# Performance work log

Measured on AMD Instinct MI355X. Metric: run time of the kernel, lower is better.

Reference implementation:

```python
import jax, jax.numpy as jnp
import numpy as np

RES, RES_, STRIDE = 28, 14, 2
H, KD, AR = 8, 16, 4
SCALE = KD ** -0.5
EPS = 1e-5


def make_bias_idxs(res=RES, res_=RES_, stride=STRIDE):
    pts = [(i, j) for i in range(res) for j in range(res)]
    pts_ = [(i, j) for i in range(res_) for j in range(res_)]
    offs, idxs = {}, []
    for p1 in pts_:
        for p2 in pts:
            off = (abs(p1[0] * stride - p2[0]), abs(p1[1] * stride - p2[1]))
            if off not in offs:
                offs[off] = len(offs)
            idxs.append(offs[off])
    return np.array(idxs, dtype=np.int32).reshape(len(pts_), len(pts)), len(offs)


def setup_inputs() -> dict:
    key = jax.random.key(0)
    ks = jax.random.split(key, 16)
    idxs, n_off = make_bias_idxs()  # n_off == 784
    B, N, C = 128, RES * RES, 256
    d_kv, d_q, d_p, d_pin = 640, 128, 384, 512
    return {
        "hidden_state": jax.random.normal(ks[0], (B, N, C), jnp.float32),
        "w_kv": jax.random.normal(ks[1], (d_kv, C), jnp.float32) * 0.05,
        "kv_gamma": jax.random.uniform(ks[2], (d_kv,), jnp.float32, 0.5, 1.5),
        "kv_beta": jax.random.normal(ks[3], (d_kv,), jnp.float32) * 0.1,
        "kv_mean": jax.random.normal(ks[4], (d_kv,), jnp.float32) * 0.1,
        "kv_var": jax.random.uniform(ks[5], (d_kv,), jnp.float32, 0.5, 1.5),
        "w_q": jax.random.normal(ks[6], (d_q, C), jnp.float32) * 0.05,
        "q_gamma": jax.random.uniform(ks[7], (d_q,), jnp.float32, 0.5, 1.5),
        "q_beta": jax.random.normal(ks[8], (d_q,), jnp.float32) * 0.1,
        "q_mean": jax.random.normal(ks[9], (d_q,), jnp.float32) * 0.1,
        "q_var": jax.random.uniform(ks[10], (d_q,), jnp.float32, 0.5, 1.5),
        "w_proj": jax.random.normal(ks[11], (d_p, d_pin), jnp.float32) * 0.05,
        "p_gamma": jax.random.uniform(ks[12], (d_p,), jnp.float32, 0.5, 1.5),
        "p_beta": jax.random.normal(ks[13], (d_p,), jnp.float32) * 0.1,
        "p_mean": jax.random.normal(ks[14], (d_p,), jnp.float32) * 0.1,
        "p_var": jax.random.uniform(ks[15], (d_p,), jnp.float32, 0.5, 1.5),
        "attention_biases": jax.random.normal(jax.random.fold_in(key, 99), (H, n_off), jnp.float32),
        "attention_bias_idxs": jnp.asarray(idxs),
    }


def _bn(x, gamma, beta, mean, var):
    # eval-mode BatchNorm1d over last dim
    return (x - mean) * (gamma * jax.lax.rsqrt(var + EPS)) + beta


def _hardswish(x):
    return x * jnp.clip(x + 3.0, 0.0, 6.0) * (1.0 / 6.0)


def reference(hidden_state, w_kv, kv_gamma, kv_beta, kv_mean, kv_var,
              w_q, q_gamma, q_beta, q_mean, q_var,
              w_proj, p_gamma, p_beta, p_mean, p_var,
              attention_biases, attention_bias_idxs):
    B, N, C = hidden_state.shape
    N_ = RES_ * RES_
    # kv: [B, N, 640] -> key [B,H,N,KD], value [B,H,N,AR*KD]
    kv = _bn(hidden_state @ w_kv.T, kv_gamma, kv_beta, kv_mean, kv_var)
    kv = kv.reshape(B, N, H, KD + AR * KD)
    k = jnp.transpose(kv[..., :KD], (0, 2, 1, 3))          # [B,H,N,KD]
    v = jnp.transpose(kv[..., KD:], (0, 2, 1, 3))          # [B,H,N,AR*KD]
    # strided query subsample on the spatial grid
    hs = hidden_state.reshape(B, RES, RES, C)[:, ::STRIDE, ::STRIDE].reshape(B, N_, C)
    q = _bn(hs @ w_q.T, q_gamma, q_beta, q_mean, q_var)
    q = jnp.transpose(q.reshape(B, N_, H, KD), (0, 2, 1, 3))  # [B,H,N_,KD]
    bias = attention_biases[:, attention_bias_idxs]           # [H,N_,N] gathered
    attn = jnp.einsum('bhqd,bhkd->bhqk', q, k) * SCALE + bias
    attn = jax.nn.softmax(attn, axis=-1)
    out = jnp.einsum('bhqk,bhkd->bhqd', attn, v)              # [B,H,N_,AR*KD]
    out = jnp.transpose(out, (0, 2, 1, 3)).reshape(B, N_, H * AR * KD)
    out = _bn(_hardswish(out) @ w_proj.T, p_gamma, p_beta, p_mean, p_var)
    return out
```

## Files before the change

### kernel.cpp

```cpp
#include <hip/hip_runtime.h>

typedef _Float16 f16;
typedef __attribute__((ext_vector_type(2))) _Float16 f16x2;
typedef __attribute__((ext_vector_type(4))) _Float16 f16x4;
typedef __attribute__((ext_vector_type(8))) _Float16 f16x8;
typedef __attribute__((ext_vector_type(4))) float fvec4;
typedef __attribute__((ext_vector_type(4))) float f32x4;
typedef __attribute__((ext_vector_type(16))) float f32x16;
typedef __attribute__((ext_vector_type(4))) unsigned int uint4v;

#define NKEY 784
#define NKEYP 800
#define NQ 196
#define NQP 224
#define LOG2E 1.442695041f
#define SC2   0.360673760f
#define THR2  11.5415603f

static __device__ __forceinline__ f32x4 mfma16(f16x8 a, f16x8 b, f32x4 c) {
    return __builtin_amdgcn_mfma_f32_16x16x32_f16(a, b, c, 0, 0, 0);
}
static __device__ __forceinline__ f32x16 mfma32(f16x8 a, f16x8 b, f32x16 c) {
    return __builtin_amdgcn_mfma_f32_32x32x16_f16(a, b, c, 0, 0, 0);
}
static __device__ __forceinline__ unsigned pkrtz(float a, float b) {
    return __builtin_bit_cast(unsigned, __builtin_amdgcn_cvt_pkrtz(a, b));
}
static __device__ __forceinline__ f32x16 z16() {
    f32x16 v;
#pragma unroll
    for (int i = 0; i < 16; ++i) v[i] = 0.f;
    return v;
}
static __device__ __forceinline__ f32x16 load_ci(const float* p) {
    fvec4 c0 = *(const fvec4*)(p);
    fvec4 c1 = *(const fvec4*)(p + 256);
    fvec4 c2 = *(const fvec4*)(p + 512);
    fvec4 c3 = *(const fvec4*)(p + 768);
    f32x16 ci;
    ci[0] = c0[0];  ci[1] = c0[1];  ci[2] = c0[2];  ci[3] = c0[3];
    ci[4] = c1[0];  ci[5] = c1[1];  ci[6] = c1[2];  ci[7] = c1[3];
    ci[8] = c2[0];  ci[9] = c2[1];  ci[10] = c2[2]; ci[11] = c2[3];
    ci[12] = c3[0]; ci[13] = c3[1]; ci[14] = c3[2]; ci[15] = c3[3];
    return ci;
}

__global__ void prep_scales_all(const float* __restrict__ kg, const float* __restrict__ kb,
                                const float* __restrict__ km, const float* __restrict__ kvv,
                                const float* __restrict__ qg, const float* __restrict__ qb,
                                const float* __restrict__ qm, const float* __restrict__ qv,
                                const float* __restrict__ pg, const float* __restrict__ pb,
                                const float* __restrict__ pm, const float* __restrict__ pv,
                                float* __restrict__ sb) {
    int i = blockIdx.x * 256 + threadIdx.x;
    if (i < 640) {
        float s = kg[i] * rsqrtf(kvv[i] + 1e-5f);
        sb[i] = s; sb[640 + i] = kb[i] - km[i] * s;
    } else if (i < 768) {
        int j = i - 640;
        float s = qg[j] * rsqrtf(qv[j] + 1e-5f);
        sb[1280 + j] = s * SC2;
        sb[1408 + j] = (qb[j] - qm[j] * s) * SC2;
    } else if (i < 1152) {
        int j = i - 768;
        float s = pg[j] * rsqrtf(pv[j] + 1e-5f);
        sb[1536 + j] = s; sb[1920 + j] = pb[j] - pm[j] * s;
    }
}

__global__ void conv_w(const float* __restrict__ wkv, const float* __restrict__ wq,
                       const float* __restrict__ wp, f16* __restrict__ out) {
    int i = blockIdx.x * 256 + threadIdx.x;
    const float* src;
    f16* dst;
    int kc, n, K;
    if (i < 20480)      { int j = i;         kc = j / 640, n = j - kc * 640; src = wkv; dst = out + (size_t)j * 8;            K = 256; }
    else if (i < 24576) { int j = i - 20480; kc = j / 128, n = j - kc * 128; src = wq;  dst = out + 163840 + (size_t)j * 8;   K = 256; }
    else                { int j = i - 24576; kc = j / 384, n = j - kc * 384; src = wp;  dst = out + 196608 + (size_t)j * 8;   K = 512; }
    const float* s = src + (size_t)n * K + kc * 8;
    fvec4 v0 = *(const fvec4*)s;
    fvec4 v1 = *(const fvec4*)(s + 4);
    f16x8 h;
    h[0] = (f16)v0[0]; h[1] = (f16)v0[1]; h[2] = (f16)v0[2]; h[3] = (f16)v0[3];
    h[4] = (f16)v1[0]; h[5] = (f16)v1[1]; h[6] = (f16)v1[2]; h[7] = (f16)v1[3];
    *(f16x8*)dst = h;
}

__global__ void prep_bias(const float* __restrict__ biases, const int* __restrict__ idxs,
                          float* __restrict__ biasC, int n_off) {
    int tid = blockIdx.x * 256 + threadIdx.x;
    const int rj = tid & 3;
    const int lane = (tid >> 2) & 63;
    const int rr = (tid >> 8) & 3;
    const int g = tid >> 10;
    const int r = rr * 4 + rj;
    const int kbk = g % 25;
    const int tmp = g / 25;
    const int qt = tmp % 7;
    const int h = tmp / 7;
    const int q = qt * 32 + (lane & 31);
    const int key = kbk * 32 + (r & 3) + 8 * (r >> 2) + 4 * (lane >> 5);
    float v;
    if (key >= NKEY)  v = -1e30f;
    else if (q < NQ)  v = biases[h * n_off + idxs[q * NKEY + key]] * LOG2E;
    else              v = 0.f;
    biasC[tid] = v;
}

template <int MODE>
__global__ __launch_bounds__(256) void gemm_db(
        const void* __restrict__ Ap, const f16x8* __restrict__ Wg,
        const float* __restrict__ sc, const float* __restrict__ sh,
        void* __restrict__ OutA, f16* __restrict__ OutV) {
    constexpr int K     = (MODE == 2) ? 512 : 256;
    constexpr int KS    = K / 32;
    constexpr int CHUNK = (MODE == 2) ? 16 : 32;
    constexpr int NFR   = CHUNK / 16;
    constexpr int NT    = (MODE == 0) ? 640 : (MODE == 1 ? 128 : 384);
    constexpr int NCH   = (MODE == 0) ? 20 : (MODE == 1 ? 4 : 12);
    constexpr int UNITS = (K / 8) * CHUNK;
    constexpr int SR    = UNITS / 256;

    __shared__ f16x8 Wl[2][UNITS];

    const int t = threadIdx.x;
    const int lane = t & 63, wid = t >> 6;
    const int fr = lane & 15, kg = lane >> 4;
    const int m0 = blockIdx.x * 64;
    const int nb0 = blockIdx.y * (NCH * CHUNK);
    const int mrow = m0 + wid * 16 + fr;

    size_t arow;
    if constexpr (MODE == 1) {
        int b = mrow / 196, nn = mrow - b * 196;
        arow = (size_t)b * 784 + (nn / 14) * 56 + (nn % 14) * 2;
    } else {
        arow = (size_t)mrow;
    }
    f16x8 af[KS];
#pragma unroll
    for (int ks = 0; ks < KS; ++ks) {
        if constexpr (MODE == 2) {
            af[ks] = *(const f16x8*)((const f16*)Ap + arow * K + ks * 32 + kg * 8);
        } else {
            const float* a = (const float*)Ap + arow * 256 + ks * 32 + kg * 8;
            fvec4 v0 = *(const fvec4*)a;
            fvec4 v1 = *(const fvec4*)(a + 4);
            f16x8 hv;
            hv[0] = (f16)v0[0]; hv[1] = (f16)v0[1]; hv[2] = (f16)v0[2]; hv[3] = (f16)v0[3];
            hv[4] = (f16)v1[0]; hv[5] = (f16)v1[1]; hv[6] = (f16)v1[2]; hv[7] = (f16)v1[3];
            af[ks] = hv;
        }
    }

#pragma unroll
    for (int rr = 0; rr < SR; ++rr) {
        const int idx = rr * 256 + t;
        Wl[0][idx] = Wg[(size_t)(idx / CHUNK) * NT + nb0 + (idx % CHUNK)];
    }
    __syncthreads();

    const int rg = kg * 4;
    int cur = 0;
    for (int c = 0; c < NCH; ++c) {
        const int n0c = nb0 + c * CHUNK;

        f16x8 nx0, nx1, nx2, nx3;
        if (c + 1 < NCH) {
            const int n0n = n0c + CHUNK;
            nx0 = Wg[(size_t)((0 * 256 + t) / CHUNK) * NT + n0n + ((0 * 256 + t) % CHUNK)];
            if constexpr (SR > 1)
                nx1 = Wg[(size_t)((1 * 256 + t) / CHUNK) * NT + n0n + ((1 * 256 + t) % CHUNK)];
            if constexpr (SR > 2) {
                nx2 = Wg[(size_t)((2 * 256 + t) / CHUNK) * NT + n0n + ((2 * 256 + t) % CHUNK)];
                nx3 = Wg[(size_t)((3 * 256 + t) / CHUNK) * NT + n0n + ((3 * 256 + t) % CHUNK)];
            }
        }

        f32x4 acc[NFR];
#pragma unroll
        for (int j = 0; j < NFR; ++j) acc[j] = (f32x4){0.f, 0.f, 0.f, 0.f};
#pragma unroll
        for (int ks = 0; ks < KS; ++ks) {
            f16x8 bfr[NFR];
#pragma unroll
            for (int nf = 0; nf < NFR; ++nf)
                bfr[nf] = Wl[cur][(ks * 4 + kg) * CHUNK + nf * 16 + fr];
#pragma unroll
            for (int nf = 0; nf < NFR; ++nf)
                acc[nf] = mfma16(af[ks], bfr[nf], acc[nf]);
        }

        const int mbase = m0 + wid * 16 + rg;
#pragma unroll
        for (int nf = 0; nf < NFR; ++nf) {
            const int n = n0c + nf * 16 + fr;
            const float scn = sc[n], shn = sh[n];
            if constexpr (MODE == 0) {
                const int b = mbase / 784;
                const int nn = mbase - b * 784;
                const int hd = n / 80;
                const int cc = n - hd * 80;
                const size_t bh = (size_t)(b * 8 + hd);
                if (cc < 16) {
#pragma unroll
                    for (int r = 0; r < 4; ++r) {
                        float y = acc[nf][r] * scn + shn;
                        ((f16*)OutA)[(bh * NKEYP + nn + r) * 16 + cc] = (f16)y;
                    }
                } else {
                    const int kbk = nn >> 5, sH = (nn >> 4) & 1;
                    const int kq = (nn >> 2) & 3;
                    const int slot = ((((kq & 1) << 1) | (kq >> 1)) << 2) | (nn & 3);
                    f16x4 pv;
#pragma unroll
                    for (int r = 0; r < 4; ++r) pv[r] = (f16)(acc[nf][r] * scn + shn);
                    *(f16x4*)(OutV + ((bh * 25 + kbk) * 2 + sH) * 1024 + (cc - 16) * 16 + slot) = pv;
                }
            } else if constexpr (MODE == 1) {
                const int b = mbase / 196;
                const int nn = mbase - b * 196;
                const int hd = n >> 4, cc = n & 15;
                const size_t bh = (size_t)(b * 8 + hd);
#pragma unroll
                for (int r = 0; r < 4; ++r) {
                    float y = acc[nf][r] * scn + shn;
                    ((f16*)OutA)[(bh * NQP + nn + r) * 16 + cc] = (f16)y;
                }
            } else {
#pragma unroll
                for (int r = 0; r < 4; ++r) {
                    float y = acc[nf][r] * scn + shn;
                    ((float*)OutA)[(size_t)(mbase + r) * 384 + n] = y;
                }
            }
        }

        if (c + 1 < NCH) {
            Wl[cur ^ 1][0 * 256 + t] = nx0;
            if constexpr (SR > 1)
                Wl[cur ^ 1][1 * 256 + t] = nx1;
            if constexpr (SR > 2) {
                Wl[cur ^ 1][2 * 256 + t] = nx2;
                Wl[cur ^ 1][3 * 256 + t] = nx3;
            }
            __syncthreads();
            cur ^= 1;
        }
    }
}

__global__ __launch_bounds__(64) void attn_fused(const f16* __restrict__ kb,
                                                 const f16* __restrict__ vtb,
                                                 const f16* __restrict__ qw,
                                                 const float* __restrict__ biasC,
                                                 f16* __restrict__ ao) {
    const int wg = blockIdx.x;
    const int x = wg & 7, p = wg >> 3;
    const int qt = p % 7;
    const int bh = (p / 7) * 8 + x;
    const int b = bh >> 3, h = bh & 7;
    const int lane = threadIdx.x;
    const int l31 = lane & 31;
    const int hh = lane >> 5;
    const int q0 = qt * 32;

    const f16x8 bq = *(const f16x8*)(qw + ((size_t)bh * NQP + q0 + l31) * 16 + hh * 8);
    const f16*   kpp = kb + (size_t)bh * (NKEYP * 16) + (size_t)l31 * 16 + hh * 8;
    const float* cbp = biasC + (size_t)(h * 7 + qt) * 25 * 1024 + lane * 4;
    const f16*   vkb = vtb + (size_t)bh * 51200 + l31 * 16 + hh * 8;

    float mrun = -1e30f;
    float lsum = 0.f;
    f32x16 o0 = z16(), o1 = z16();

    f32x16 sn = mfma32(*(const f16x8*)kpp, bq, load_ci(cbp));

#pragma unroll 1
    for (int kbi = 0; kbi < 25; ++kbi) {
        f32x16 s = sn;
        if (kbi + 1 < 25) {
            kpp += 512; cbp += 1024;
            sn = mfma32(*(const f16x8*)kpp, bq, load_ci(cbp));
        }
        f16x8 bv00 = *(const f16x8*)(vkb);
        f16x8 bv01 = *(const f16x8*)(vkb + 512);
        f16x8 bv10 = *(const f16x8*)(vkb + 1024);
        f16x8 bv11 = *(const f16x8*)(vkb + 1536);
        vkb += 2048;

        float m0v = fmaxf(fmaxf(s[0], s[1]), fmaxf(s[2], s[3]));
        float m1v = fmaxf(fmaxf(s[4], s[5]), fmaxf(s[6], s[7]));
        float m2v = fmaxf(fmaxf(s[8], s[9]), fmaxf(s[10], s[11]));
        float m3v = fmaxf(fmaxf(s[12], s[13]), fmaxf(s[14], s[15]));
        float cmax = fmaxf(fmaxf(m0v, m1v), fmaxf(m2v, m3v));
        cmax = fmaxf(cmax, __shfl_xor(cmax, 32));
        if (__any(cmax > mrun + THR2)) {
            float mnew = fmaxf(mrun, cmax);
            float f = exp2f(mrun - mnew);
            mrun = mnew;
            lsum *= f;
#pragma unroll
            for (int r = 0; r < 16; ++r) {
                const int cr = (r & 3) + ((r >> 2) << 3) + (hh << 2);
                float fr2 = __shfl(f, cr);
                o0[r] *= fr2;
                o1[r] *= fr2;
            }
        }
        float pr[16];
        float psum = 0.f;
#pragma unroll
        for (int r = 0; r < 16; ++r) {
            pr[r] = exp2f(s[r] - mrun);
            psum += pr[r];
        }
        lsum += psum;
        uint4v w0, w1;
        w0[0] = pkrtz(pr[0], pr[1]);   w0[1] = pkrtz(pr[2], pr[3]);
        w0[2] = pkrtz(pr[4], pr[5]);   w0[3] = pkrtz(pr[6], pr[7]);
        w1[0] = pkrtz(pr[8], pr[9]);   w1[1] = pkrtz(pr[10], pr[11]);
        w1[2] = pkrtz(pr[12], pr[13]); w1[3] = pkrtz(pr[14], pr[15]);
        f16x8 pa0 = __builtin_bit_cast(f16x8, w0);
        f16x8 pa1 = __builtin_bit_cast(f16x8, w1);
        o0 = mfma32(pa0, bv00, o0);
        o1 = mfma32(pa0, bv01, o1);
        o0 = mfma32(pa1, bv10, o0);
        o1 = mfma32(pa1, bv11, o1);
    }
    lsum += __shfl_xor(lsum, 32);
    const float inv = 1.0f / lsum;
#pragma unroll
    for (int r = 0; r < 16; ++r) {
        const int cr = (r & 3) + ((r >> 2) << 3) + (hh << 2);
        const float iq = __shfl(inv, cr);
        const int qg = q0 + cr;
        if (qg < NQ) {
            float v0 = o0[r] * iq, v1 = o1[r] * iq;
            float h0 = v0 * fminf(fmaxf(v0 + 3.f, 0.f), 6.f) * (1.f / 6.f);
            float h1 = v1 * fminf(fmaxf(v1 + 3.f, 0.f), 6.f) * (1.f / 6.f);
            f16* dst = ao + ((size_t)b * NQ + qg) * 512 + h * 64 + l31;
            dst[0] = (f16)h0;
            dst[32] = (f16)h1;
        }
    }
}

extern "C" void kernel_launch(void* const* d_in, const int* in_sizes, int n_in,
                              void* d_out, int out_size, void* d_ws, size_t ws_size,
                              hipStream_t stream) {
    (void)n_in; (void)out_size;
    const float* hidden = (const float*)d_in[0];
    const float* w_kv   = (const float*)d_in[1];
    const float* w_q    = (const float*)d_in[6];
    const float* w_p    = (const float*)d_in[11];
    const float* biases = (const float*)d_in[16];
    const int*   idxs   = (const int*)d_in[17];
    const int n_off = in_sizes[16] / 8;

    char* ws = (char*)d_ws;
    const size_t OFF_K  = 0;
    const size_t OFF_V  = 26214400;
    const size_t OFF_Q  = 131072000;
    const size_t OFF_AO = 138412032;
    const size_t OFF_W  = 164102144;
    const size_t OFF_SC = 164888576;
    const size_t OFF_BT = 164897792;
    const size_t NEED   = OFF_BT + 5734400;
    f16*   kbuf  = (f16*)(ws + OFF_K);
    f16*   vbuf  = (f16*)(ws + OFF_V);
    f16*   qbuf  = (f16*)(ws + OFF_Q);
    f16*   aobuf = (f16*)(ws + OFF_AO);
    f16*   wf16  = (f16*)(ws + OFF_W);
    float* scbuf = (float*)(ws + OFF_SC);
    float* btbuf = (ws_size >= NEED) ? (float*)(ws + OFF_BT) : (float*)d_out;

    prep_scales_all<<<5, 256, 0, stream>>>(
        (const float*)d_in[2], (const float*)d_in[3], (const float*)d_in[4], (const float*)d_in[5],
        (const float*)d_in[7], (const float*)d_in[8], (const float*)d_in[9], (const float*)d_in[10],
        (const float*)d_in[12], (const float*)d_in[13], (const float*)d_in[14], (const float*)d_in[15],
        scbuf);
    conv_w<<<192, 256, 0, stream>>>(w_kv, w_q, w_p, wf16);
    prep_bias<<<5600, 256, 0, stream>>>(biases, idxs, btbuf, n_off);
    hipMemsetAsync(qbuf, 0, (size_t)1024 * NQP * 16 * 2, stream);
    gemm_db<0><<<dim3(1568, 1), 256, 0, stream>>>(hidden, (const f16x8*)wf16, scbuf, scbuf + 640, kbuf, vbuf);
    gemm_db<1><<<dim3(392, 1), 256, 0, stream>>>(hidden, (const f16x8*)(wf16 + 163840), scbuf + 1280, scbuf + 1408, qbuf, nullptr);
    attn_fused<<<7168, 64, 0, stream>>>(kbuf, vbuf, qbuf, btbuf, aobuf);
    gemm_db<2><<<dim3(392, 2), 256, 0, stream>>>(aobuf, (const f16x8*)(wf16 + 196608), scbuf + 1536, scbuf + 1920, d_out, nullptr);
}
```

Before: 226.9 us.

## Store attention bias as fp16 and run all query tiles of a head in one block

The precomputed bias table becomes fp16 with a per-lane contiguous layout, so each lane loads it as two 16-byte vectors instead of four strided float4 loads, halving bias traffic. The attention kernel now launches one 448-thread block per batch-head, with seven waves covering the query tiles, so K and V loads for a head are shared through cache within a block. The fp16 bias loses precision, and the padding mask value changes to -30000. The fallback that wrote the bias table into the output buffer when workspace was small is removed.

```diff
diff --git a/kernel.cpp b/kernel.cpp
--- a/kernel.cpp
+++ b/kernel.cpp
@@ -31,18 +31,6 @@
 #pragma unroll
     for (int i = 0; i < 16; ++i) v[i] = 0.f;
     return v;
-}
-static __device__ __forceinline__ f32x16 load_ci(const float* p) {
-    fvec4 c0 = *(const fvec4*)(p);
-    fvec4 c1 = *(const fvec4*)(p + 256);
-    fvec4 c2 = *(const fvec4*)(p + 512);
-    fvec4 c3 = *(const fvec4*)(p + 768);
-    f32x16 ci;
-    ci[0] = c0[0];  ci[1] = c0[1];  ci[2] = c0[2];  ci[3] = c0[3];
-    ci[4] = c1[0];  ci[5] = c1[1];  ci[6] = c1[2];  ci[7] = c1[3];
-    ci[8] = c2[0];  ci[9] = c2[1];  ci[10] = c2[2]; ci[11] = c2[3];
-    ci[12] = c3[0]; ci[13] = c3[1]; ci[14] = c3[2]; ci[15] = c3[3];
-    return ci;
 }
 
 __global__ void prep_scales_all(const float* __restrict__ kg, const float* __restrict__ kb,
@@ -87,13 +75,11 @@
 }
 
 __global__ void prep_bias(const float* __restrict__ biases, const int* __restrict__ idxs,
-                          float* __restrict__ biasC, int n_off) {
+                          f16* __restrict__ biasS, int n_off) {
     int tid = blockIdx.x * 256 + threadIdx.x;
-    const int rj = tid & 3;
-    const int lane = (tid >> 2) & 63;
-    const int rr = (tid >> 8) & 3;
+    const int r = tid & 15;
+    const int lane = (tid >> 4) & 63;
     const int g = tid >> 10;
-    const int r = rr * 4 + rj;
     const int kbk = g % 25;
     const int tmp = g / 25;
     const int qt = tmp % 7;
@@ -101,10 +87,10 @@
     const int q = qt * 32 + (lane & 31);
     const int key = kbk * 32 + (r & 3) + 8 * (r >> 2) + 4 * (lane >> 5);
     float v;
-    if (key >= NKEY)  v = -1e30f;
+    if (key >= NKEY)  v = -30000.f;
     else if (q < NQ)  v = biases[h * n_off + idxs[q * NKEY + key]] * LOG2E;
     else              v = 0.f;
-    biasC[tid] = v;
+    biasS[tid] = (f16)v;
 }
 
 template <int MODE>
@@ -250,38 +236,49 @@
     }
 }
 
-__global__ __launch_bounds__(64) void attn_fused(const f16* __restrict__ kb,
-                                                 const f16* __restrict__ vtb,
-                                                 const f16* __restrict__ qw,
-                                                 const float* __restrict__ biasC,
-                                                 f16* __restrict__ ao) {
-    const int wg = blockIdx.x;
-    const int x = wg & 7, p = wg >> 3;
-    const int qt = p % 7;
-    const int bh = (p / 7) * 8 + x;
+__global__ __launch_bounds__(448) void attn_fused(const f16* __restrict__ kb,
+                                                  const f16* __restrict__ vtb,
+                                                  const f16* __restrict__ qw,
+                                                  const f16* __restrict__ biasS,
+                                                  f16* __restrict__ ao) {
+    const int bh = blockIdx.x;
     const int b = bh >> 3, h = bh & 7;
-    const int lane = threadIdx.x;
+    const int wid = threadIdx.x >> 6;
+    const int lane = threadIdx.x & 63;
     const int l31 = lane & 31;
     const int hh = lane >> 5;
-    const int q0 = qt * 32;
+    const int q0 = wid * 32;
 
     const f16x8 bq = *(const f16x8*)(qw + ((size_t)bh * NQP + q0 + l31) * 16 + hh * 8);
-    const f16*   kpp = kb + (size_t)bh * (NKEYP * 16) + (size_t)l31 * 16 + hh * 8;
-    const float* cbp = biasC + (size_t)(h * 7 + qt) * 25 * 1024 + lane * 4;
-    const f16*   vkb = vtb + (size_t)bh * 51200 + l31 * 16 + hh * 8;
+    const f16* kpp = kb + (size_t)bh * (NKEYP * 16) + (size_t)l31 * 16 + hh * 8;
+    const f16* cbp = biasS + ((size_t)(h * 7 + wid) * 25 * 64 + lane) * 16;
+    const f16* vkb = vtb + (size_t)bh * 51200 + l31 * 16 + hh * 8;
 
     float mrun = -1e30f;
     float lsum = 0.f;
     f32x16 o0 = z16(), o1 = z16();
 
-    f32x16 sn = mfma32(*(const f16x8*)kpp, bq, load_ci(cbp));
+    f32x16 sn;
+    {
+        const f16x8* bp = (const f16x8*)cbp;
+        f16x8 b0 = bp[0], b1 = bp[1];
+        f32x16 ci;
+#pragma unroll
+        for (int r = 0; r < 8; ++r) { ci[r] = (float)b0[r]; ci[8 + r] = (float)b1[r]; }
+        sn = mfma32(*(const f16x8*)kpp, bq, ci);
+    }
 
 #pragma unroll 1
     for (int kbi = 0; kbi < 25; ++kbi) {
         f32x16 s = sn;
         if (kbi + 1 < 25) {
             kpp += 512; cbp += 1024;
-            sn = mfma32(*(const f16x8*)kpp, bq, load_ci(cbp));
+            const f16x8* bp = (const f16x8*)cbp;
+            f16x8 b0 = bp[0], b1 = bp[1];
+            f32x16 ci;
+#pragma unroll
+            for (int r = 0; r < 8; ++r) { ci[r] = (float)b0[r]; ci[8 + r] = (float)b1[r]; }
+            sn = mfma32(*(const f16x8*)kpp, bq, ci);
         }
         f16x8 bv00 = *(const f16x8*)(vkb);
         f16x8 bv01 = *(const f16x8*)(vkb + 512);
@@ -349,7 +346,7 @@
 extern "C" void kernel_launch(void* const* d_in, const int* in_sizes, int n_in,
                               void* d_out, int out_size, void* d_ws, size_t ws_size,
                               hipStream_t stream) {
-    (void)n_in; (void)out_size;
+    (void)n_in; (void)out_size; (void)ws_size;
     const float* hidden = (const float*)d_in[0];
     const float* w_kv   = (const float*)d_in[1];
     const float* w_q    = (const float*)d_in[6];
@@ -366,14 +363,13 @@
     const size_t OFF_W  = 164102144;
     const size_t OFF_SC = 164888576;
     const size_t OFF_BT = 164897792;
-    const size_t NEED   = OFF_BT + 5734400;
     f16*   kbuf  = (f16*)(ws + OFF_K);
     f16*   vbuf  = (f16*)(ws + OFF_V);
     f16*   qbuf  = (f16*)(ws + OFF_Q);
     f16*   aobuf = (f16*)(ws + OFF_AO);
     f16*   wf16  = (f16*)(ws + OFF_W);
     float* scbuf = (float*)(ws + OFF_SC);
-    float* btbuf = (ws_size >= NEED) ? (float*)(ws + OFF_BT) : (float*)d_out;
+    f16*   btbuf = (f16*)(ws + OFF_BT);
 
     prep_scales_all<<<5, 256, 0, stream>>>(
         (const float*)d_in[2], (const float*)d_in[3], (const float*)d_in[4], (const float*)d_in[5],
@@ -385,6 +381,6 @@
     hipMemsetAsync(qbuf, 0, (size_t)1024 * NQP * 16 * 2, stream);
     gemm_db<0><<<dim3(1568, 1), 256, 0, stream>>>(hidden, (const f16x8*)wf16, scbuf, scbuf + 640, kbuf, vbuf);
     gemm_db<1><<<dim3(392, 1), 256, 0, stream>>>(hidden, (const f16x8*)(wf16 + 163840), scbuf + 1280, scbuf + 1408, qbuf, nullptr);
-    attn_fused<<<7168, 64, 0, stream>>>(kbuf, vbuf, qbuf, btbuf, aobuf);
+    attn_fused<<<1024, 448, 0, stream>>>(kbuf, vbuf, qbuf, btbuf, aobuf);
     gemm_db<2><<<dim3(392, 2), 256, 0, stream>>>(aobuf, (const f16x8*)(wf16 + 196608), scbuf + 1536, scbuf + 1920, d_out, nullptr);
 }
```

New measurement: 210.6 us. 1.08x faster.
